# Kernel optimization log

Hardware: AMD Instinct MI355X
Metric: run time of the kernel (lower is better)

## Reference

```python
import jax, jax.numpy as jnp
import numpy as np

B, C, VC, H, W = 4, 256, 128, 64, 64


def setup_inputs() -> dict:
    key = jax.random.key(0)
    kx, kq, kk, kv = jax.random.split(key, 4)
    # Conv2d 1x1 no-bias weights are just [out_channels, in_channels] matrices.
    s = 1.0 / np.sqrt(C)
    return {
        "x": jax.random.normal(kx, (B, C, H, W), dtype=jnp.float32),
        "Wq": jax.random.uniform(kq, (VC, C), minval=-s, maxval=s, dtype=jnp.float32),
        "Wk": jax.random.uniform(kk, (VC, C), minval=-s, maxval=s, dtype=jnp.float32),
        "Wv": jax.random.uniform(kv, (VC, C), minval=-s, maxval=s, dtype=jnp.float32),
    }


def reference(x, Wq, Wk, Wv):
    # 1x1 convs == per-pixel channel GEMMs
    Q = jnp.einsum('bchw,dc->bdhw', x, Wq)  # [B, VC, H, W]
    K = jnp.einsum('bchw,dc->bdhw', x, Wk)
    V = jnp.einsum('bchw,dc->bdhw', x, Wv)
    b, d, h, w = Q.shape
    # affinity over all spatial pairs: [B, H, W, H, W]
    aff = jnp.einsum('bdij,bdkl->bijkl', Q, K).reshape(b, h, w, h * w)
    aff = jax.nn.softmax(aff, axis=3).reshape(b, h, w, h, w)
    # attention-weighted aggregation of values
    out = jnp.einsum('bijkl,bdkl->bdij', aff, V)  # [B, VC, H, W]
    return out
```

## Files before the change

### kernel.cpp

```cpp
#include <hip/hip_runtime.h>
#include <hip/hip_bf16.h>

#define B_ 4
#define C_ 256
#define D_ 128
#define N_ 4096

typedef float f32x4 __attribute__((ext_vector_type(4)));
typedef short bf16x8 __attribute__((ext_vector_type(8)));
typedef short s16x4 __attribute__((ext_vector_type(4)));
typedef unsigned short u16;
typedef unsigned int u32;

__device__ __forceinline__ u16 f2bf(float f) {
  unsigned u = __float_as_uint(f);
  u += 0x7fffu + ((u >> 16) & 1u);
  return (u16)(u >> 16);
}
__device__ __forceinline__ float bf2f(u16 v) {
  return __uint_as_float(((u32)v) << 16);
}
__device__ __forceinline__ u32 cvt_pk_bf16(float a, float b) {
  u32 r;
  asm("v_cvt_pk_bf16_f32 %0, %1, %2" : "=v"(r) : "v"(a), "v"(b));
  return r;
}

__global__ __launch_bounds__(256) void castw_kernel(
    const float* __restrict__ Wq, const float* __restrict__ Wk,
    const float* __restrict__ Wv, u16* __restrict__ Whi,
    u16* __restrict__ Wlo) {
  const int i = blockIdx.x * 256 + threadIdx.x;
  const int m = i >> 13;
  const int j = (i & 8191) * 4;
  const float* src = (m == 0) ? Wq : (m == 1) ? Wk : Wv;
  const float scale = (m == 0) ? 1.44269504f : 1.0f;
  const float4 v = *(const float4*)(src + j);
  const float vv[4] = {v.x * scale, v.y * scale, v.z * scale, v.w * scale};
  s16x4 h, l;
#pragma unroll
  for (int k = 0; k < 4; ++k) {
    const u16 hb = f2bf(vv[k]);
    h[k] = (short)hb;
    l[k] = (short)f2bf(vv[k] - bf2f(hb));
  }
  *(s16x4*)&Whi[m * 32768 + j] = h;
  *(s16x4*)&Wlo[m * 32768 + j] = l;
}

__global__ __launch_bounds__(256, 2) void proj_kernel(
    const float* __restrict__ x, const u16* __restrict__ Whi,
    const u16* __restrict__ Wlo, u16* __restrict__ Qo, u16* __restrict__ Ko,
    u16* __restrict__ Vt) {
  __shared__ __align__(16) u16 xs_h[32 * 256];
  __shared__ __align__(16) u16 xs_l[32 * 256];

  const int n0 = blockIdx.x * 32;
  const int b = blockIdx.y;
  const int t = threadIdx.x;
  const int w = t >> 6, lane = t & 63, g = lane >> 4, c = lane & 15;

  {
    const float* xb = x + ((size_t)b * C_) * N_ + n0;
#pragma unroll
    for (int r = 0; r < 8; ++r) {
      const int id = r * 256 + t;
      const int cr = id >> 3, nq = (id & 7) * 4;
      const float4 v = *(const float4*)(xb + (size_t)cr * N_ + nq);
      const float vv[4] = {v.x, v.y, v.z, v.w};
#pragma unroll
      for (int k2 = 0; k2 < 4; ++k2) {
        const int idx2 = (nq + k2) * 256 + (cr ^ (((nq + k2) & 7) << 3));
        const u16 hb = f2bf(vv[k2]);
        xs_h[idx2] = hb;
        xs_l[idx2] = f2bf(vv[k2] - bf2f(hb));
      }
    }
  }
  __syncthreads();

  if (w < 2) {
    const size_t wo = (size_t)w * 32768;
    u16* __restrict__ O = (w == 0 ? Qo : Ko) + (size_t)b * N_ * D_;
#pragma unroll 1
    for (int dt = 0; dt < 8; ++dt) {
      bf16x8 wfh[8], wfl[8];
#pragma unroll
      for (int kc = 0; kc < 8; ++kc) {
        const size_t off = wo + (size_t)(dt * 16 + c) * 256 + kc * 32 + g * 8;
        wfh[kc] = *(const bf16x8*)&Whi[off];
        wfl[kc] = *(const bf16x8*)&Wlo[off];
      }
#pragma unroll
      for (int nt = 0; nt < 2; ++nt) {
        f32x4 a = {0.f, 0.f, 0.f, 0.f};
#pragma unroll
        for (int kc = 0; kc < 8; ++kc) {
          const int xi = (nt * 16 + c) * 256 +
                         ((kc * 32 + g * 8) ^ ((c & 7) << 3));
          const bf16x8 xh = *(const bf16x8*)&xs_h[xi];
          const bf16x8 xl = *(const bf16x8*)&xs_l[xi];
          a = __builtin_amdgcn_mfma_f32_16x16x32_bf16(xh, wfh[kc], a, 0, 0, 0);
          a = __builtin_amdgcn_mfma_f32_16x16x32_bf16(xh, wfl[kc], a, 0, 0, 0);
          a = __builtin_amdgcn_mfma_f32_16x16x32_bf16(xl, wfh[kc], a, 0, 0, 0);
        }
#pragma unroll
        for (int i = 0; i < 4; ++i)
          O[(size_t)(n0 + nt * 16 + g * 4 + i) * D_ + dt * 16 + c] = f2bf(a[i]);
      }
    }
  } else {
    const size_t wo = (size_t)2 * 32768;
    const int d0 = (w - 2) * 64;
    u16* __restrict__ O = Vt + (size_t)b * D_ * N_;
#pragma unroll 1
    for (int dt = 0; dt < 4; ++dt) {
      bf16x8 wfh[8], wfl[8];
#pragma unroll
      for (int kc = 0; kc < 8; ++kc) {
        const size_t off =
            wo + (size_t)(d0 + dt * 16 + c) * 256 + kc * 32 + g * 8;
        wfh[kc] = *(const bf16x8*)&Whi[off];
        wfl[kc] = *(const bf16x8*)&Wlo[off];
      }
#pragma unroll
      for (int nt = 0; nt < 2; ++nt) {
        f32x4 a = {0.f, 0.f, 0.f, 0.f};
#pragma unroll
        for (int kc = 0; kc < 8; ++kc) {
          const int xi = (nt * 16 + c) * 256 +
                         ((kc * 32 + g * 8) ^ ((c & 7) << 3));
          const bf16x8 xh = *(const bf16x8*)&xs_h[xi];
          const bf16x8 xl = *(const bf16x8*)&xs_l[xi];
          a = __builtin_amdgcn_mfma_f32_16x16x32_bf16(wfh[kc], xh, a, 0, 0, 0);
          a = __builtin_amdgcn_mfma_f32_16x16x32_bf16(wfl[kc], xh, a, 0, 0, 0);
          a = __builtin_amdgcn_mfma_f32_16x16x32_bf16(wfh[kc], xl, a, 0, 0, 0);
        }
#pragma unroll
        for (int i = 0; i < 4; ++i)
          O[(size_t)(d0 + dt * 16 + g * 4 + i) * N_ + n0 + nt * 16 + c] =
              f2bf(a[i]);
      }
    }
  }
}

__device__ __forceinline__ int kIdx(int row, int col) {
  return row * 128 + (col ^ ((row & 7) << 3));
}
__device__ __forceinline__ int vIdx(int d, int col) {
  return d * 64 + (col ^ ((d & 7) << 3));
}
__device__ __forceinline__ int kprm(int q) {
  const int ct = q >> 2, qq = q & 3;
  return ((ct >> 1) << 5) +
         (((qq >> 1) == (ct & 1)) ? (qq << 3) : (((qq ^ 2) << 3) + 4));
}

__global__ __launch_bounds__(256, 2) void attn_kernel(
    const u16* __restrict__ Q, const u16* __restrict__ K,
    const u16* __restrict__ Vt, u16* __restrict__ op,
    float* __restrict__ mb, float* __restrict__ lb,
    float* __restrict__ outf, int qt, int rem, int S) {
  __shared__ __align__(16) u16 lds_k[64 * 128];
  __shared__ __align__(16) u16 lds_vt[128 * 64];

  const int L = blockIdx.x;
  int qx, b, sid;
  if (((B_ * S) & 7) == 0) {
    const int gpx = (B_ * S) >> 3;
    const int xcd = L & 7, idx = L >> 3;
    const int grp = xcd * gpx + (idx >> 5);
    qx = idx & 31;
    b = grp / S;
    sid = grp - b * S;
  } else {
    qx = L & 31;
    const int r2 = L >> 5;
    b = r2 % B_;
    sid = r2 / B_;
  }
  const int q0 = qx * 128;
  const int NT = qt + (sid < rem ? 1 : 0);
  const int t0 = sid * qt + (sid < rem ? sid : rem);
  const int k0 = t0 * 64;
  const int t = threadIdx.x;
  const int w = t >> 6, lane = t & 63, g = lane >> 4, c = lane & 15;
  const int qw = q0 + w * 32;
  const bool ghi = (g & 2) != 0;

  const u16* __restrict__ Qb = Q + (size_t)b * N_ * D_;
  const u16* __restrict__ Kb = K + (size_t)b * N_ * D_;
  const u16* __restrict__ Vb = Vt + (size_t)b * D_ * N_;

  bf16x8 qf[2][4];
#pragma unroll
  for (int qh = 0; qh < 2; ++qh)
#pragma unroll
    for (int kc = 0; kc < 4; ++kc)
      qf[qh][kc] =
          *(const bf16x8*)&Qb[(size_t)(qw + qh * 16 + c) * D_ + kc * 32 + g * 8];

  f32x4 acc[8][2];
  f32x4 accl[2];
#pragma unroll
  for (int dt = 0; dt < 8; ++dt)
#pragma unroll
    for (int qh = 0; qh < 2; ++qh) acc[dt][qh] = (f32x4){0.f, 0.f, 0.f, 0.f};
  accl[0] = (f32x4){0.f, 0.f, 0.f, 0.f};
  accl[1] = (f32x4){0.f, 0.f, 0.f, 0.f};
  float mrow[2] = {-3.0e38f, -3.0e38f};
  const float THR = 11.5415603f;

  bf16x8 onesv;
#pragma unroll
  for (int j = 0; j < 8; ++j) onesv[j] = (short)0x3F80;

  bf16x8 krg[4], vrg[4];
  auto load_tile = [&](int kbase) {
#pragma unroll
    for (int i = 0; i < 4; ++i) {
      const int idx = i * 256 + t;
      krg[i] = *(const bf16x8*)&Kb[(size_t)(kbase + (idx >> 4)) * D_ + (idx & 15) * 8];
      vrg[i] = *(const bf16x8*)&Vb[(size_t)(idx >> 3) * N_ + kbase + (idx & 7) * 8];
    }
  };
  load_tile(k0);

  for (int kt = 0; kt < NT; ++kt) {
    __syncthreads();
#pragma unroll
    for (int i = 0; i < 4; ++i) {
      const int idx = i * 256 + t;
      *(bf16x8*)&lds_k[kIdx(idx >> 4, (idx & 15) * 8)] = krg[i];
      const int d = idx >> 3, rc = idx & 7;
      s16x4 lo, hi;
      lo[0] = vrg[i][0]; lo[1] = vrg[i][1]; lo[2] = vrg[i][2]; lo[3] = vrg[i][3];
      hi[0] = vrg[i][4]; hi[1] = vrg[i][5]; hi[2] = vrg[i][6]; hi[3] = vrg[i][7];
      *(s16x4*)&lds_vt[vIdx(d, kprm(rc * 2))] = lo;
      *(s16x4*)&lds_vt[vIdx(d, kprm(rc * 2 + 1))] = hi;
    }
    if (kt + 1 < NT) load_tile(k0 + (kt + 1) * 64);
    __syncthreads();

    f32x4 s[4][2];
#pragma unroll
    for (int ct = 0; ct < 4; ++ct)
#pragma unroll
      for (int qh = 0; qh < 2; ++qh) s[ct][qh] = (f32x4){0.f, 0.f, 0.f, 0.f};
    __builtin_amdgcn_s_setprio(1);
#pragma unroll
    for (int kc = 0; kc < 4; ++kc) {
#pragma unroll
      for (int ct = 0; ct < 4; ++ct) {
        const bf16x8 kf =
            *(const bf16x8*)&lds_k[kIdx(ct * 16 + c, kc * 32 + g * 8)];
        s[ct][0] = __builtin_amdgcn_mfma_f32_16x16x32_bf16(kf, qf[0][kc], s[ct][0], 0, 0, 0);
        s[ct][1] = __builtin_amdgcn_mfma_f32_16x16x32_bf16(kf, qf[1][kc], s[ct][1], 0, 0, 0);
      }
    }
    __builtin_amdgcn_s_setprio(0);

    float pml[2];
#pragma unroll
    for (int qh = 0; qh < 2; ++qh) {
      const float m0 = fmaxf(fmaxf(s[0][qh][0], s[0][qh][1]),
                             fmaxf(s[0][qh][2], s[0][qh][3]));
      const float m1 = fmaxf(fmaxf(s[1][qh][0], s[1][qh][1]),
                             fmaxf(s[1][qh][2], s[1][qh][3]));
      const float m2 = fmaxf(fmaxf(s[2][qh][0], s[2][qh][1]),
                             fmaxf(s[2][qh][2], s[2][qh][3]));
      const float m3 = fmaxf(fmaxf(s[3][qh][0], s[3][qh][1]),
                             fmaxf(s[3][qh][2], s[3][qh][3]));
      pml[qh] = fmaxf(fmaxf(m0, m1), fmaxf(m2, m3));
    }
    const bool need =
        __any((pml[0] > mrow[0] + THR) || (pml[1] > mrow[1] + THR));
    if (need) {
#pragma unroll
      for (int qh = 0; qh < 2; ++qh) {
        float p = pml[qh];
        p = fmaxf(p, __shfl_xor(p, 16));
        p = fmaxf(p, __shfl_xor(p, 32));
        const float mnew = fmaxf(mrow[qh], p);
        const float scl = exp2f(mrow[qh] - mnew);
        mrow[qh] = mnew;
        accl[qh][0] *= scl; accl[qh][1] *= scl;
        accl[qh][2] *= scl; accl[qh][3] *= scl;
#pragma unroll
        for (int dt = 0; dt < 8; ++dt) {
          acc[dt][qh][0] *= scl; acc[dt][qh][1] *= scl;
          acc[dt][qh][2] *= scl; acc[dt][qh][3] *= scl;
        }
      }
    }
#pragma unroll
    for (int qh = 0; qh < 2; ++qh)
#pragma unroll
      for (int ct = 0; ct < 4; ++ct)
#pragma unroll
        for (int i = 0; i < 4; ++i)
          s[ct][qh][i] = exp2f(s[ct][qh][i] - mrow[qh]);

    u32 pfw[2][2][4];
#pragma unroll
    for (int kc = 0; kc < 2; ++kc) {
#pragma unroll
      for (int qh = 0; qh < 2; ++qh) {
        const u32 lo0 = cvt_pk_bf16(s[kc * 2][qh][0], s[kc * 2][qh][1]);
        const u32 lo1 = cvt_pk_bf16(s[kc * 2][qh][2], s[kc * 2][qh][3]);
        const u32 hi0 = cvt_pk_bf16(s[kc * 2 + 1][qh][0], s[kc * 2 + 1][qh][1]);
        const u32 hi1 = cvt_pk_bf16(s[kc * 2 + 1][qh][2], s[kc * 2 + 1][qh][3]);
        pfw[kc][qh][0] = ghi ? hi0 : lo0;
        pfw[kc][qh][1] = ghi ? hi1 : lo1;
        const u32 s0 = ghi ? lo0 : hi0;
        const u32 s1 = ghi ? lo1 : hi1;
        pfw[kc][qh][2] = (u32)__shfl_xor((int)s0, 32);
        pfw[kc][qh][3] = (u32)__shfl_xor((int)s1, 32);
      }
    }

#pragma unroll
    for (int kc = 0; kc < 2; ++kc) {
      union { u32 w[4]; bf16x8 v; } u0, u1;
#pragma unroll
      for (int j = 0; j < 4; ++j) { u0.w[j] = pfw[kc][0][j]; u1.w[j] = pfw[kc][1][j]; }
      __builtin_amdgcn_s_setprio(1);
      accl[0] = __builtin_amdgcn_mfma_f32_16x16x32_bf16(onesv, u0.v, accl[0], 0, 0, 0);
      accl[1] = __builtin_amdgcn_mfma_f32_16x16x32_bf16(onesv, u1.v, accl[1], 0, 0, 0);
#pragma unroll
      for (int dt = 0; dt < 8; ++dt) {
        const bf16x8 vf =
            *(const bf16x8*)&lds_vt[vIdx(dt * 16 + c, kc * 32 + g * 8)];
        acc[dt][0] = __builtin_amdgcn_mfma_f32_16x16x32_bf16(vf, u0.v, acc[dt][0], 0, 0, 0);
        acc[dt][1] = __builtin_amdgcn_mfma_f32_16x16x32_bf16(vf, u1.v, acc[dt][1], 0, 0, 0);
      }
      __builtin_amdgcn_s_setprio(0);
    }
  }

#pragma unroll
  for (int qh = 0; qh < 2; ++qh) {
    const int n = qw + qh * 16 + c;
    const float lr = accl[qh][0];
    if (mb) {
      u16* __restrict__ ob = op + ((size_t)(sid * B_ + b) * D_) * N_;
#pragma unroll
      for (int dt = 0; dt < 8; ++dt)
#pragma unroll
        for (int i = 0; i < 4; ++i)
          ob[(size_t)(dt * 16 + g * 4 + i) * N_ + n] = f2bf(acc[dt][qh][i]);
      if (g == 0) {
        mb[(size_t)(sid * B_ + b) * N_ + n] = mrow[qh];
        lb[(size_t)(sid * B_ + b) * N_ + n] = lr;
      }
    } else {
      const float linv = 1.0f / lr;
      float* __restrict__ ob = outf + (size_t)b * D_ * N_;
#pragma unroll
      for (int dt = 0; dt < 8; ++dt)
#pragma unroll
        for (int i = 0; i < 4; ++i)
          ob[(size_t)(dt * 16 + g * 4 + i) * N_ + n] = acc[dt][qh][i] * linv;
    }
  }
}

__global__ __launch_bounds__(256) void combine_kernel(
    const u16* __restrict__ op, const float* __restrict__ mbu,
    const float* __restrict__ lbu, float* __restrict__ out, int S) {
  const int idx = blockIdx.x * 256 + threadIdx.x;
  const int n0 = (idx & (N_ / 4 - 1)) * 4;
  const int bd = idx >> 10;
  const int b = bd >> 7, d = bd & (D_ - 1);

  float4 msv[8], lsv[8];
  float M0 = -3e38f, M1 = -3e38f, M2 = -3e38f, M3 = -3e38f;
#pragma unroll
  for (int s = 0; s < 8; ++s)
    if (s < S) {
      msv[s] = *(const float4*)&mbu[(size_t)(s * B_ + b) * N_ + n0];
      lsv[s] = *(const float4*)&lbu[(size_t)(s * B_ + b) * N_ + n0];
      M0 = fmaxf(M0, msv[s].x); M1 = fmaxf(M1, msv[s].y);
      M2 = fmaxf(M2, msv[s].z); M3 = fmaxf(M3, msv[s].w);
    }
  float d0 = 0.f, d1 = 0.f, d2 = 0.f, d3 = 0.f;
  float a0 = 0.f, a1 = 0.f, a2 = 0.f, a3 = 0.f;
#pragma unroll
  for (int s = 0; s < 8; ++s)
    if (s < S) {
      const float w0 = exp2f(msv[s].x - M0);
      const float w1 = exp2f(msv[s].y - M1);
      const float w2 = exp2f(msv[s].z - M2);
      const float w3 = exp2f(msv[s].w - M3);
      d0 += lsv[s].x * w0; d1 += lsv[s].y * w1;
      d2 += lsv[s].z * w2; d3 += lsv[s].w * w3;
      const s16x4 o =
          *(const s16x4*)&op[((size_t)(s * B_ + b) * D_ + d) * N_ + n0];
      a0 += w0 * bf2f((u16)o[0]); a1 += w1 * bf2f((u16)o[1]);
      a2 += w2 * bf2f((u16)o[2]); a3 += w3 * bf2f((u16)o[3]);
    }
  float4 r = {a0 / d0, a1 / d1, a2 / d2, a3 / d3};
  *(float4*)&out[((size_t)b * D_ + d) * N_ + n0] = r;
}

extern "C" void kernel_launch(void* const* d_in, const int* in_sizes, int n_in,
                              void* d_out, int out_size, void* d_ws, size_t ws_size,
                              hipStream_t stream) {
  const float* x  = (const float*)d_in[0];
  const float* Wq = (const float*)d_in[1];
  const float* Wk = (const float*)d_in[2];
  const float* Wv = (const float*)d_in[3];
  float* out = (float*)d_out;

  u16* whi  = (u16*)d_ws;
  u16* wlo  = whi + (size_t)3 * 128 * 256;
  u16* q_ws = wlo + (size_t)3 * 128 * 256;
  u16* k_ws = q_ws + (size_t)B_ * N_ * D_;
  u16* v_ws = k_ws + (size_t)B_ * N_ * D_;

  castw_kernel<<<96, 256, 0, stream>>>(Wq, Wk, Wv, whi, wlo);
  proj_kernel<<<dim3(N_ / 32, B_), 256, 0, stream>>>(x, whi, wlo, q_ws, k_ws,
                                                     v_ws);

  const size_t baseB =
      ((size_t)6 * 128 * 256 + (size_t)3 * B_ * N_ * D_) * 2;
  int S = 0;
  const int cands[4] = {6, 4, 2, 1};
  for (int ci = 0; ci < 4; ++ci) {
    const int cand = cands[ci];
    const size_t need = baseB + (size_t)cand * ((size_t)B_ * D_ * N_ * 2 +
                                                (size_t)2 * B_ * N_ * 4);
    if (ws_size >= need) { S = cand; break; }
  }
  if (S > 1) {
    u16* opb = (u16*)((char*)d_ws + baseB);
    float* mbuf = (float*)(opb + (size_t)S * B_ * D_ * N_);
    float* lbuf = mbuf + (size_t)S * B_ * N_;
    attn_kernel<<<dim3(32 * B_ * S), 256, 0, stream>>>(
        q_ws, k_ws, v_ws, opb, mbuf, lbuf, nullptr, 64 / S, 64 % S, S);
    combine_kernel<<<(B_ * D_ * N_ / 4) / 256, 256, 0, stream>>>(opb, mbuf,
                                                                 lbuf, out, S);
  } else {
    attn_kernel<<<dim3(32 * B_), 256, 0, stream>>>(
        q_ws, k_ws, v_ws, nullptr, nullptr, nullptr, out, 64, 0, 1);
  }
}
```

Before: 101.9 us.

## Split projection output channels across grid z and interleave two MFMA chains

Launches the projection kernel with a third grid dimension of 2 so each block computes half of the output channels, doubling the block count. Each block still converts the full x tile into shared memory, so that load and conversion work is duplicated across the two z-halves. The inner loop now runs both 16-row n-tiles together as two independent accumulators, which gives more MFMA parallelism. Weight fragments are loaded in halves to cut register pressure, and launch bounds are raised to 3 blocks per CU to allow more occupancy.

```diff
diff --git a/kernel.cpp b/kernel.cpp
--- a/kernel.cpp
+++ b/kernel.cpp
@@ -48,7 +48,7 @@
   *(s16x4*)&Wlo[m * 32768 + j] = l;
 }
 
-__global__ __launch_bounds__(256, 2) void proj_kernel(
+__global__ __launch_bounds__(256, 3) void proj_kernel(
     const float* __restrict__ x, const u16* __restrict__ Whi,
     const u16* __restrict__ Wlo, u16* __restrict__ Qo, u16* __restrict__ Ko,
     u16* __restrict__ Vt) {
@@ -57,6 +57,7 @@
 
   const int n0 = blockIdx.x * 32;
   const int b = blockIdx.y;
+  const int z = blockIdx.z;
   const int t = threadIdx.x;
   const int w = t >> 6, lane = t & 63, g = lane >> 4, c = lane & 15;
 
@@ -83,63 +84,81 @@
     const size_t wo = (size_t)w * 32768;
     u16* __restrict__ O = (w == 0 ? Qo : Ko) + (size_t)b * N_ * D_;
 #pragma unroll 1
-    for (int dt = 0; dt < 8; ++dt) {
-      bf16x8 wfh[8], wfl[8];
-#pragma unroll
-      for (int kc = 0; kc < 8; ++kc) {
-        const size_t off = wo + (size_t)(dt * 16 + c) * 256 + kc * 32 + g * 8;
-        wfh[kc] = *(const bf16x8*)&Whi[off];
-        wfl[kc] = *(const bf16x8*)&Wlo[off];
-      }
-#pragma unroll
-      for (int nt = 0; nt < 2; ++nt) {
-        f32x4 a = {0.f, 0.f, 0.f, 0.f};
-#pragma unroll
-        for (int kc = 0; kc < 8; ++kc) {
-          const int xi = (nt * 16 + c) * 256 +
-                         ((kc * 32 + g * 8) ^ ((c & 7) << 3));
-          const bf16x8 xh = *(const bf16x8*)&xs_h[xi];
-          const bf16x8 xl = *(const bf16x8*)&xs_l[xi];
-          a = __builtin_amdgcn_mfma_f32_16x16x32_bf16(xh, wfh[kc], a, 0, 0, 0);
-          a = __builtin_amdgcn_mfma_f32_16x16x32_bf16(xh, wfl[kc], a, 0, 0, 0);
-          a = __builtin_amdgcn_mfma_f32_16x16x32_bf16(xl, wfh[kc], a, 0, 0, 0);
+    for (int dti = 0; dti < 4; ++dti) {
+      const int dt = z * 4 + dti;
+      f32x4 a0 = {0.f, 0.f, 0.f, 0.f};
+      f32x4 a1 = {0.f, 0.f, 0.f, 0.f};
+#pragma unroll 1
+      for (int kcb = 0; kcb < 2; ++kcb) {
+        bf16x8 wfh[4], wfl[4];
+#pragma unroll
+        for (int j = 0; j < 4; ++j) {
+          const size_t off = wo + (size_t)(dt * 16 + c) * 256 +
+                             (kcb * 4 + j) * 32 + g * 8;
+          wfh[j] = *(const bf16x8*)&Whi[off];
+          wfl[j] = *(const bf16x8*)&Wlo[off];
         }
 #pragma unroll
-        for (int i = 0; i < 4; ++i)
-          O[(size_t)(n0 + nt * 16 + g * 4 + i) * D_ + dt * 16 + c] = f2bf(a[i]);
+        for (int j = 0; j < 4; ++j) {
+          const int kc = kcb * 4 + j;
+          const int col = (kc * 32 + g * 8) ^ ((c & 7) << 3);
+          const bf16x8 xh0 = *(const bf16x8*)&xs_h[c * 256 + col];
+          const bf16x8 xl0 = *(const bf16x8*)&xs_l[c * 256 + col];
+          const bf16x8 xh1 = *(const bf16x8*)&xs_h[(16 + c) * 256 + col];
+          const bf16x8 xl1 = *(const bf16x8*)&xs_l[(16 + c) * 256 + col];
+          a0 = __builtin_amdgcn_mfma_f32_16x16x32_bf16(xh0, wfh[j], a0, 0, 0, 0);
+          a0 = __builtin_amdgcn_mfma_f32_16x16x32_bf16(xh0, wfl[j], a0, 0, 0, 0);
+          a0 = __builtin_amdgcn_mfma_f32_16x16x32_bf16(xl0, wfh[j], a0, 0, 0, 0);
+          a1 = __builtin_amdgcn_mfma_f32_16x16x32_bf16(xh1, wfh[j], a1, 0, 0, 0);
+          a1 = __builtin_amdgcn_mfma_f32_16x16x32_bf16(xh1, wfl[j], a1, 0, 0, 0);
+          a1 = __builtin_amdgcn_mfma_f32_16x16x32_bf16(xl1, wfh[j], a1, 0, 0, 0);
+        }
+      }
+#pragma unroll
+      for (int i = 0; i < 4; ++i) {
+        O[(size_t)(n0 + g * 4 + i) * D_ + dt * 16 + c] = f2bf(a0[i]);
+        O[(size_t)(n0 + 16 + g * 4 + i) * D_ + dt * 16 + c] = f2bf(a1[i]);
       }
     }
   } else {
     const size_t wo = (size_t)2 * 32768;
-    const int d0 = (w - 2) * 64;
+    const int d0 = (w - 2) * 64 + z * 32;
     u16* __restrict__ O = Vt + (size_t)b * D_ * N_;
 #pragma unroll 1
-    for (int dt = 0; dt < 4; ++dt) {
-      bf16x8 wfh[8], wfl[8];
-#pragma unroll
-      for (int kc = 0; kc < 8; ++kc) {
-        const size_t off =
-            wo + (size_t)(d0 + dt * 16 + c) * 256 + kc * 32 + g * 8;
-        wfh[kc] = *(const bf16x8*)&Whi[off];
-        wfl[kc] = *(const bf16x8*)&Wlo[off];
-      }
-#pragma unroll
-      for (int nt = 0; nt < 2; ++nt) {
-        f32x4 a = {0.f, 0.f, 0.f, 0.f};
-#pragma unroll
-        for (int kc = 0; kc < 8; ++kc) {
-          const int xi = (nt * 16 + c) * 256 +
-                         ((kc * 32 + g * 8) ^ ((c & 7) << 3));
-          const bf16x8 xh = *(const bf16x8*)&xs_h[xi];
-          const bf16x8 xl = *(const bf16x8*)&xs_l[xi];
-          a = __builtin_amdgcn_mfma_f32_16x16x32_bf16(wfh[kc], xh, a, 0, 0, 0);
-          a = __builtin_amdgcn_mfma_f32_16x16x32_bf16(wfl[kc], xh, a, 0, 0, 0);
-          a = __builtin_amdgcn_mfma_f32_16x16x32_bf16(wfh[kc], xl, a, 0, 0, 0);
+    for (int dti = 0; dti < 2; ++dti) {
+      const int dr = d0 + dti * 16;
+      f32x4 a0 = {0.f, 0.f, 0.f, 0.f};
+      f32x4 a1 = {0.f, 0.f, 0.f, 0.f};
+#pragma unroll 1
+      for (int kcb = 0; kcb < 2; ++kcb) {
+        bf16x8 wfh[4], wfl[4];
+#pragma unroll
+        for (int j = 0; j < 4; ++j) {
+          const size_t off =
+              wo + (size_t)(dr + c) * 256 + (kcb * 4 + j) * 32 + g * 8;
+          wfh[j] = *(const bf16x8*)&Whi[off];
+          wfl[j] = *(const bf16x8*)&Wlo[off];
         }
 #pragma unroll
-        for (int i = 0; i < 4; ++i)
-          O[(size_t)(d0 + dt * 16 + g * 4 + i) * N_ + n0 + nt * 16 + c] =
-              f2bf(a[i]);
+        for (int j = 0; j < 4; ++j) {
+          const int kc = kcb * 4 + j;
+          const int col = (kc * 32 + g * 8) ^ ((c & 7) << 3);
+          const bf16x8 xh0 = *(const bf16x8*)&xs_h[c * 256 + col];
+          const bf16x8 xl0 = *(const bf16x8*)&xs_l[c * 256 + col];
+          const bf16x8 xh1 = *(const bf16x8*)&xs_h[(16 + c) * 256 + col];
+          const bf16x8 xl1 = *(const bf16x8*)&xs_l[(16 + c) * 256 + col];
+          a0 = __builtin_amdgcn_mfma_f32_16x16x32_bf16(wfh[j], xh0, a0, 0, 0, 0);
+          a0 = __builtin_amdgcn_mfma_f32_16x16x32_bf16(wfl[j], xh0, a0, 0, 0, 0);
+          a0 = __builtin_amdgcn_mfma_f32_16x16x32_bf16(wfh[j], xl0, a0, 0, 0, 0);
+          a1 = __builtin_amdgcn_mfma_f32_16x16x32_bf16(wfh[j], xh1, a1, 0, 0, 0);
+          a1 = __builtin_amdgcn_mfma_f32_16x16x32_bf16(wfl[j], xh1, a1, 0, 0, 0);
+          a1 = __builtin_amdgcn_mfma_f32_16x16x32_bf16(wfh[j], xl1, a1, 0, 0, 0);
+        }
+      }
+#pragma unroll
+      for (int i = 0; i < 4; ++i) {
+        O[(size_t)(dr + g * 4 + i) * N_ + n0 + c] = f2bf(a0[i]);
+        O[(size_t)(dr + g * 4 + i) * N_ + n0 + 16 + c] = f2bf(a1[i]);
       }
     }
   }
@@ -420,8 +439,8 @@
   u16* v_ws = k_ws + (size_t)B_ * N_ * D_;
 
   castw_kernel<<<96, 256, 0, stream>>>(Wq, Wk, Wv, whi, wlo);
-  proj_kernel<<<dim3(N_ / 32, B_), 256, 0, stream>>>(x, whi, wlo, q_ws, k_ws,
-                                                     v_ws);
+  proj_kernel<<<dim3(N_ / 32, B_, 2), 256, 0, stream>>>(x, whi, wlo, q_ws,
+                                                        k_ws, v_ws);
 
   const size_t baseB =
       ((size_t)6 * 128 * 256 + (size_t)3 * B_ * N_ * D_) * 2;
```

Result: no change. 101.6 us (-0.3%).
